# Kernel tuning notes

Hardware: AMD Instinct MI355X
Metric: run time of the kernel (lower is better)

The kernel has to match this reference:

```python
import jax, jax.numpy as jnp
import numpy as np

N_HEAD, CTX, N_EMBD, HEAD_SIZE = 16, 2048, 1024, 64
D_MODEL = N_HEAD * HEAD_SIZE  # 1024


def setup_inputs() -> dict:
    key = jax.random.key(0)
    ks = jax.random.split(key, 8)
    s_in = 1.0 / np.sqrt(N_EMBD)
    s_d = 1.0 / np.sqrt(D_MODEL)
    s_ff = 1.0 / np.sqrt(4 * D_MODEL)
    return {
        "x": jax.random.normal(ks[0], (4, CTX, N_EMBD), dtype=jnp.float32),
        # per-head q/k/v projections stacked over heads: [H, n_embd, head_size]
        "Wq": jax.random.normal(ks[1], (N_HEAD, N_EMBD, HEAD_SIZE), dtype=jnp.float32) * s_in,
        "Wk": jax.random.normal(ks[2], (N_HEAD, N_EMBD, HEAD_SIZE), dtype=jnp.float32) * s_in,
        "Wv": jax.random.normal(ks[3], (N_HEAD, N_EMBD, HEAD_SIZE), dtype=jnp.float32) * s_in,
        # FFN: Linear(d, 4d) -> Linear(4d, d) -> ReLU (dropout = identity in eval)
        "W1": jax.random.normal(ks[4], (D_MODEL, 4 * D_MODEL), dtype=jnp.float32) * s_d,
        "b1": jnp.zeros((4 * D_MODEL,), dtype=jnp.float32),
        "W2": jax.random.normal(ks[5], (4 * D_MODEL, D_MODEL), dtype=jnp.float32) * s_ff,
        "b2": jnp.zeros((D_MODEL,), dtype=jnp.float32),
    }


def reference(x, Wq, Wk, Wv, W1, b1, W2, b2):
    B, T, C = x.shape
    scale = 1.0 / np.sqrt(HEAD_SIZE)
    # project: [B,T,C] x [H,C,D] -> [B,H,T,D]
    q = jnp.einsum('btc,hcd->bhtd', x, Wq)
    k = jnp.einsum('btc,hcd->bhtd', x, Wk)
    v = jnp.einsum('btc,hcd->bhtd', x, Wv)
    # causal attention scores [B,H,T,T]
    wei = jnp.einsum('bhtd,bhsd->bhts', q, k) * scale
    causal = jnp.tril(jnp.ones((T, T), dtype=bool))
    wei = jnp.where(causal, wei, -jnp.inf)
    wei = jax.nn.softmax(wei, axis=-1)
    out = jnp.einsum('bhts,bhsd->bhtd', wei, v)
    # concat heads -> [B,T,H*D]
    out = out.transpose(0, 2, 1, 3).reshape(B, T, D_MODEL)
    # FFN: note original applies ReLU AFTER the second linear
    h = out @ W1 + b1
    h = h @ W2 + b2
    return jax.nn.relu(h)
```

## Files before the change

kernel.cpp:

```cpp
#include <hip/hip_runtime.h>
#include <hip/hip_bf16.h>

typedef unsigned short u16;
typedef unsigned int u32;
typedef short bf16x8 __attribute__((ext_vector_type(8)));
typedef float floatx4 __attribute__((ext_vector_type(4)));

#define CTX 2048
#define HEADSZ 64
#define NHEAD 16
#define DMODEL 1024
#define DFF 4096
#define MROWS 8192
#define C_SCALE 0.18033688011112042f

__device__ __forceinline__ u16 f2b(float f) {
  union { float f; u32 i; } x; x.f = f;
  u32 i = x.i;
  return (u16)((i + 0x7fffu + ((i >> 16) & 1u)) >> 16);
}
__device__ __forceinline__ u32 pack2(float a, float b) {
  return (u32)f2b(a) | ((u32)f2b(b) << 16);
}
__device__ __forceinline__ u32 cvtpk(float a, float b) {
  u32 r;
  asm("v_cvt_pk_bf16_f32 %0, %1, %2" : "=v"(r) : "v"(a), "v"(b));
  return r;
}
__device__ __forceinline__ float ex2(float x) {
#if __has_builtin(__builtin_amdgcn_exp2f)
  return __builtin_amdgcn_exp2f(x);
#else
  float r;
  asm("v_exp_f32 %0, %1" : "=v"(r) : "v"(x));
  return r;
#endif
}

__device__ __forceinline__ void gl2lds16(const u16* g, u16* l) {
  __builtin_amdgcn_global_load_lds(
      (const __attribute__((address_space(1))) void*)g,
      (__attribute__((address_space(3))) void*)l, 16, 0, 0);
}

__global__ __launch_bounds__(256) void cvt2(const float* __restrict__ x,
                                            u16* __restrict__ xb,
                                            const float* __restrict__ w1,
                                            u16* __restrict__ w1b) {
  int i = (blockIdx.x * 256 + threadIdx.x) * 4;
  if (i < MROWS * 1024) {
    float4 v = *(const float4*)(x + i);
    *(uint2*)(xb + i) = make_uint2(pack2(v.x, v.y), pack2(v.z, v.w));
  } else {
    int j = i - MROWS * 1024;
    float4 v = *(const float4*)(w1 + j);
    *(uint2*)(w1b + j) = make_uint2(pack2(v.x, v.y), pack2(v.z, v.w));
  }
}

__global__ void transpose_f32_bf16(const float* __restrict__ in, u16* __restrict__ out,
                                   int R, int C, long ibs, long obs) {
  __shared__ u16 tile[32][33];
  const float* ip = in + (size_t)blockIdx.z * ibs;
  u16* op = out + (size_t)blockIdx.z * obs;
  int c0 = blockIdx.x * 32, r0 = blockIdx.y * 32;
  int tx = threadIdx.x, ty = threadIdx.y;
#pragma unroll
  for (int i = 0; i < 32; i += 8)
    tile[ty + i][tx] = f2b(ip[(size_t)(r0 + ty + i) * C + (c0 + tx)]);
  __syncthreads();
#pragma unroll
  for (int i = 0; i < 32; i += 8)
    op[(size_t)(c0 + ty + i) * R + (r0 + tx)] = tile[tx][ty + i];
}

__global__ void transpose_qkv(const float* __restrict__ Wq, const float* __restrict__ Wk,
                              const float* __restrict__ Wv, u16* __restrict__ out) {
  __shared__ u16 tile[32][33];
  int z = blockIdx.z;
  int sec = z >> 4, hh = z & 15;
  const float* ip = (sec == 0 ? Wq : sec == 1 ? Wk : Wv) + (size_t)hh * 65536;
  u16* op = out + (size_t)(sec * 16 + hh) * 65536;
  int c0 = blockIdx.x * 32, r0 = blockIdx.y * 32;
  int tx = threadIdx.x, ty = threadIdx.y;
#pragma unroll
  for (int i = 0; i < 32; i += 8)
    tile[ty + i][tx] = f2b(ip[(size_t)(r0 + ty + i) * 64 + (c0 + tx)]);
  __syncthreads();
#pragma unroll
  for (int i = 0; i < 32; i += 8)
    op[(size_t)(c0 + ty + i) * 1024 + (r0 + tx)] = tile[tx][ty + i];
}

__global__ __launch_bounds__(256) void reduce_wf(const float* __restrict__ p,
                                                 u16* __restrict__ wft) {
  int i = (blockIdx.x * 256 + threadIdx.x) * 4;
  float4 s = *(const float4*)(p + i);
#pragma unroll
  for (int sp = 1; sp < 8; sp++) {
    float4 v = *(const float4*)(p + ((size_t)sp << 20) + i);
    s.x += v.x; s.y += v.y; s.z += v.z; s.w += v.w;
  }
  *(uint2*)(wft + i) = make_uint2(pack2(s.x, s.y), pack2(s.z, s.w));
}

__global__ __launch_bounds__(256) void bf_acc(const float* __restrict__ b1,
                                              const float* __restrict__ W2,
                                              float* __restrict__ bf) {
  int n = blockIdx.x * 256 + threadIdx.x;
  int f0 = blockIdx.y * 128;
  float s = 0.f;
  for (int f = 0; f < 128; f++) s += b1[f0 + f] * W2[(size_t)(f0 + f) * 1024 + n];
  atomicAdd(&bf[n], s);
}

template <int MODE>
__global__ __launch_bounds__(512, 4) void gemm128(
    const u16* __restrict__ A, const u16* __restrict__ Bt,
    const float* __restrict__ bias,
    void* __restrict__ o0v, void* __restrict__ o1v, void* __restrict__ o2v,
    int N, int Klen, int Kstride) {
  __shared__ __align__(16) u16 SH[32768];
  const int tid = threadIdx.x;
  const int quad = (tid >> 4) & 3, l15 = tid & 15;
  const int wave = tid >> 6;
  const int wr = wave >> 2, wc = wave & 3;

  const int id = blockIdx.x;
  int blockM, blockN, koff;
  if (MODE == 3) {
    blockM = (id & 7) << 7;
    blockN = ((id >> 3) & 3) << 8;
    koff = (id >> 5) << 9;
  } else {
    blockM = (((id & 7) << 3) | ((id >> 3) & 7)) << 7;
    blockN = (id >> 6) << 8;
    koff = 0;
  }

  const int crow = tid >> 2;
  const int cslot = (tid & 3) ^ (crow & 3);
  const u16* ap  = A + (size_t)(blockM + crow) * Kstride + koff + cslot * 8;
  const u16* bp0 = Bt + (size_t)(blockN + crow) * Kstride + koff + cslot * 8;
  const u16* bp1 = bp0 + (size_t)128 * Kstride;

  floatx4 acc[4][4];
#pragma unroll
  for (int i = 0; i < 4; i++)
#pragma unroll
    for (int j = 0; j < 4; j++) acc[i][j] = (floatx4){0.f, 0.f, 0.f, 0.f};

  const int nk = Klen >> 5;

  gl2lds16(ap, SH + tid * 8);
  gl2lds16(bp0, SH + 8192 + tid * 8);
  gl2lds16(bp1, SH + 8192 + 4096 + tid * 8);
  ap += 32; bp0 += 32; bp1 += 32;

  const int aoff = (wr * 64 + l15) * 64 + ((quad ^ (l15 & 3)) << 4);
  const int boff = (wc * 64 + l15) * 64 + ((quad ^ (l15 & 3)) << 4);

#pragma unroll 1
  for (int t = 0; t < nk; t++) {
    const int cur = t & 1, nxt = cur ^ 1;
    if (t + 1 < nk) {
      u16* An = SH + nxt * 4096;
      u16* Bn = SH + 8192 + nxt * 8192;
      gl2lds16(ap, An + tid * 8);
      gl2lds16(bp0, Bn + tid * 8);
      gl2lds16(bp1, Bn + 4096 + tid * 8);
      ap += 32; bp0 += 32; bp1 += 32;
      asm volatile("s_waitcnt vmcnt(3)" ::: "memory");
    } else {
      asm volatile("s_waitcnt vmcnt(0)" ::: "memory");
    }
    __builtin_amdgcn_s_barrier();
    const char* ab = (const char*)(SH + cur * 4096);
    const char* bb = (const char*)(SH + 8192 + cur * 8192);
    bf16x8 ar[4], br[4];
#pragma unroll
    for (int mf = 0; mf < 4; mf++)
      ar[mf] = *(const bf16x8*)(ab + mf * 1024 + aoff);
#pragma unroll
    for (int nf = 0; nf < 4; nf++)
      br[nf] = *(const bf16x8*)(bb + nf * 1024 + boff);
    asm volatile("s_waitcnt lgkmcnt(0)" ::: "memory");
    __builtin_amdgcn_s_setprio(1);
#pragma unroll
    for (int mf = 0; mf < 4; mf++)
#pragma unroll
      for (int nf = 0; nf < 4; nf++)
        acc[mf][nf] = __builtin_amdgcn_mfma_f32_16x16x32_bf16(ar[mf], br[nf], acc[mf][nf], 0, 0, 0);
    __builtin_amdgcn_s_setprio(0);
    __builtin_amdgcn_s_barrier();
  }

  const int m0 = blockM + wr * 64 + quad * 4;
  const int n0 = blockN + wc * 64 + l15;
  if (MODE == 0) {
    u16* o0 = (u16*)o0v; u16* o1 = (u16*)o1v; u16* o2 = (u16*)o2v;
    const int lane = tid & 63;
    const int n0w = blockN + wc * 64;
    const int sec = n0w >> 10, hh = (n0w >> 6) & 15;
    const int m0w = blockM + wr * 64;
    const int b = m0w >> 11, t0 = m0w & 2047;
    const int lr = lane >> 3, lc = lane & 7;
    u16* buf = SH + wave * 4096;
    if (sec < 2) {
      u16* dst = (sec == 0) ? o0 : o1;
      const float scl = (sec == 0) ? C_SCALE : 1.0f;
#pragma unroll
      for (int nf = 0; nf < 4; nf++)
#pragma unroll
        for (int mf = 0; mf < 4; mf++)
#pragma unroll
          for (int r = 0; r < 4; r++) {
            int row = mf * 16 + quad * 4 + r;
            int col2 = (nf * 16 + l15) ^ ((row & 7) << 3);
            buf[row * 64 + col2] = f2b(acc[mf][nf][r] * scl);
          }
      u16* base = dst + ((size_t)((b * 16 + hh) * 2048 + t0)) * 64 + lc * 8;
#pragma unroll
      for (int i = 0; i < 8; i++) {
        int row = i * 8 + lr;
        uint4 v = *(const uint4*)(buf + row * 64 + ((lc ^ lr) << 3));
        *(uint4*)(base + (size_t)row * 64) = v;
      }
    } else {
      u16* dstv = o2 + ((size_t)((b * 16 + hh) * 64)) * CTX + t0;
#pragma unroll
      for (int nf = 0; nf < 4; nf++)
#pragma unroll
        for (int mf = 0; mf < 4; mf++) {
          int dr = nf * 16 + l15;
          int tc = (mf * 16 + quad * 4) ^ ((dr & 7) << 3);
          *(uint2*)&buf[dr * 64 + tc] = make_uint2(
              pack2(acc[mf][nf][0], acc[mf][nf][1]),
              pack2(acc[mf][nf][2], acc[mf][nf][3]));
        }
#pragma unroll
      for (int i = 0; i < 8; i++) {
        int dr = i * 8 + lr;
        uint4 v = *(const uint4*)&buf[dr * 64 + ((lc * 8) ^ ((dr & 7) << 3))];
        *(uint4*)(dstv + (size_t)dr * CTX + lc * 8) = v;
      }
    }
  } else if (MODE == 2) {
    float* o0 = (float*)o0v;
    const float* bias2 = (const float*)o1v;
#pragma unroll
    for (int nf = 0; nf < 4; nf++) {
      int n = n0 + nf * 16;
      float bv = bias[n] + bias2[n];
#pragma unroll
      for (int mf = 0; mf < 4; mf++)
#pragma unroll
        for (int r = 0; r < 4; r++) {
          int m = m0 + mf * 16 + r;
          float v = acc[mf][nf][r] + bv;
          o0[(size_t)m * N + n] = v > 0.f ? v : 0.f;
        }
    }
  } else {
    float* o0 = (float*)o0v + ((size_t)(id >> 5) << 20);
#pragma unroll
    for (int nf = 0; nf < 4; nf++) {
      int n = n0 + nf * 16;
#pragma unroll
      for (int mf = 0; mf < 4; mf++)
#pragma unroll
        for (int r = 0; r < 4; r++) {
          int m = m0 + mf * 16 + r;
          o0[(size_t)m * N + n] = acc[mf][nf][r];
        }
    }
  }
}

__global__ __launch_bounds__(256) void attn_mfma(
    const u16* __restrict__ Q, const u16* __restrict__ K,
    const u16* __restrict__ Vt, u16* __restrict__ out) {
  __shared__ __align__(16) u16 Kbuf[2][4096];
  __shared__ __align__(16) u16 Vbuf[2][4096];
  __shared__ __align__(16) u16 Plds[4][32][72];
  const int tid = threadIdx.x;
  const int wave = tid >> 6, lane = tid & 63;
  const int quad = lane >> 4, l15 = lane & 15;
  const int sx = l15 & 7;
  const int bh = blockIdx.x;
  const int j = 15 - blockIdx.y;
  const size_t qkb = (size_t)bh * CTX * 64;
  const size_t vb = (size_t)bh * 64 * CTX;

  const int ch0 = wave * 64 + lane;
  const int ch1 = 256 + ch0;
  const int r0 = ch0 >> 3, s0 = (ch0 & 7) ^ (r0 & 7);
  const int r1 = ch1 >> 3, s1 = (ch1 & 7) ^ (r1 & 7);
  const u16* kg0 = K + qkb + r0 * 64 + s0 * 8;
  const u16* kg1 = K + qkb + r1 * 64 + s1 * 8;
  const u16* vg0 = Vt + vb + (size_t)r0 * CTX + s0 * 8;
  const u16* vg1 = Vt + vb + (size_t)r1 * CTX + s1 * 8;

  const int qbase = j * 128 + wave * 32;
  const int NST = 2 * j + 2;
  const int nstw = 2 * j + (wave >> 1) + 1;

  bf16x8 qf[2][2];
#pragma unroll
  for (int mt = 0; mt < 2; mt++)
#pragma unroll
    for (int kc = 0; kc < 2; kc++)
      qf[mt][kc] = *(const bf16x8*)(Q + qkb + (size_t)(qbase + mt * 16 + l15) * 64 + kc * 32 + quad * 8);

  bf16x8 ones;
#pragma unroll
  for (int i = 0; i < 8; i++) ones[i] = (short)0x3F80;

  floatx4 o[2][4];
#pragma unroll
  for (int mt = 0; mt < 2; mt++)
#pragma unroll
    for (int dt = 0; dt < 4; dt++) o[mt][dt] = (floatx4){0.f, 0.f, 0.f, 0.f};
  floatx4 lacc[2];
  lacc[0] = (floatx4){0.f, 0.f, 0.f, 0.f};
  lacc[1] = (floatx4){0.f, 0.f, 0.f, 0.f};

  gl2lds16(kg0, &Kbuf[0][wave * 512]);
  gl2lds16(kg1, &Kbuf[0][2048 + wave * 512]);
  gl2lds16(vg0, &Vbuf[0][wave * 512]);
  gl2lds16(vg1, &Vbuf[0][2048 + wave * 512]);

#pragma unroll 1
  for (int st = 0; st < NST; st++) {
    __syncthreads();
    if (st + 1 < NST) {
      const int sb = (st + 1) * 64;
      const int b = (st + 1) & 1;
      gl2lds16(kg0 + sb * 64, &Kbuf[b][wave * 512]);
      gl2lds16(kg1 + sb * 64, &Kbuf[b][2048 + wave * 512]);
      gl2lds16(vg0 + sb, &Vbuf[b][wave * 512]);
      gl2lds16(vg1 + sb, &Vbuf[b][2048 + wave * 512]);
    }
    if (st >= nstw) continue;
    const int sbase = st * 64;
    const u16* kb = Kbuf[st & 1];
    const u16* vv = Vbuf[st & 1];

    floatx4 stf[2][4];
    __builtin_amdgcn_s_setprio(1);
#pragma unroll
    for (int sc = 0; sc < 4; sc++) {
      const bf16x8* kr = (const bf16x8*)(kb + (sc * 16 + l15) * 64);
      bf16x8 k0 = kr[quad ^ sx];
      bf16x8 k1 = kr[(4 + quad) ^ sx];
#pragma unroll
      for (int mt = 0; mt < 2; mt++) {
        floatx4 z = (floatx4){0.f, 0.f, 0.f, 0.f};
        z = __builtin_amdgcn_mfma_f32_16x16x32_bf16(k0, qf[mt][0], z, 0, 0, 0);
        stf[mt][sc] = __builtin_amdgcn_mfma_f32_16x16x32_bf16(k1, qf[mt][1], z, 0, 0, 0);
      }
    }
    __builtin_amdgcn_s_setprio(0);
    if (st == nstw - 1) {
#pragma unroll
      for (int mt = 0; mt < 2; mt++) {
        int qq = qbase + mt * 16 + l15;
#pragma unroll
        for (int sc = 0; sc < 4; sc++)
#pragma unroll
          for (int r = 0; r < 4; r++) {
            int s = sbase + sc * 16 + quad * 4 + r;
            if (s > qq) stf[mt][sc][r] = -1e30f;
          }
      }
    }
#pragma unroll
    for (int mt = 0; mt < 2; mt++) {
#pragma unroll
      for (int sc = 0; sc < 4; sc++) {
        floatx4 s4 = stf[mt][sc];
        float p0 = ex2(s4[0]);
        float p1 = ex2(s4[1]);
        float p2 = ex2(s4[2]);
        float p3 = ex2(s4[3]);
        *(uint2*)&Plds[wave][mt * 16 + l15][sc * 16 + quad * 4] =
            make_uint2(cvtpk(p0, p1), cvtpk(p2, p3));
      }
    }
    asm volatile("s_waitcnt lgkmcnt(0)" ::: "memory");
    __builtin_amdgcn_s_setprio(1);
#pragma unroll
    for (int sc2 = 0; sc2 < 2; sc2++) {
      bf16x8 pf[2];
#pragma unroll
      for (int mt = 0; mt < 2; mt++)
        pf[mt] = *(const bf16x8*)&Plds[wave][mt * 16 + l15][sc2 * 32 + quad * 8];
#pragma unroll
      for (int mt = 0; mt < 2; mt++)
        lacc[mt] = __builtin_amdgcn_mfma_f32_16x16x32_bf16(ones, pf[mt], lacc[mt], 0, 0, 0);
#pragma unroll
      for (int dt = 0; dt < 4; dt++) {
        const bf16x8* vr = (const bf16x8*)(vv + (dt * 16 + l15) * 64);
        bf16x8 vf = vr[(sc2 * 4 + quad) ^ sx];
#pragma unroll
        for (int mt = 0; mt < 2; mt++)
          o[mt][dt] = __builtin_amdgcn_mfma_f32_16x16x32_bf16(vf, pf[mt], o[mt][dt], 0, 0, 0);
      }
    }
    __builtin_amdgcn_s_setprio(0);
  }

#pragma unroll
  for (int mt = 0; mt < 2; mt++) {
    float inv = 1.0f / lacc[mt][0];
    int row = (bh >> 4) * CTX + qbase + mt * 16 + l15;
    u16* orow = out + (size_t)row * DMODEL + (bh & 15) * 64;
#pragma unroll
    for (int dt = 0; dt < 4; dt++) {
      floatx4 v = o[mt][dt];
      *(u32*)(orow + dt * 16 + quad * 4) = cvtpk(v[0] * inv, v[1] * inv);
      *(u32*)(orow + dt * 16 + quad * 4 + 2) = cvtpk(v[2] * inv, v[3] * inv);
    }
  }
}

extern "C" void kernel_launch(void* const* d_in, const int* in_sizes, int n_in,
                              void* d_out, int out_size, void* d_ws, size_t ws_size,
                              hipStream_t stream) {
  const float* x  = (const float*)d_in[0];
  const float* Wq = (const float*)d_in[1];
  const float* Wk = (const float*)d_in[2];
  const float* Wv = (const float*)d_in[3];
  const float* W1 = (const float*)d_in[4];
  const float* b1 = (const float*)d_in[5];
  const float* W2 = (const float*)d_in[6];
  const float* b2 = (const float*)d_in[7];
  float* out = (float*)d_out;

  u16* ws    = (u16*)d_ws;
  u16* W2t   = ws;
  u16* W1b   = W2t + (size_t)1024 * 4096;
  u16* Wft   = W1b + (size_t)1024 * 4096;
  float* bfv = (float*)(Wft + (size_t)1024 * 1024);
  u16* xb    = Wft + (size_t)1024 * 1024 + 4096;
  u16* Wqkvt = xb + (size_t)MROWS * 1024;
  u16* q     = Wqkvt + (size_t)3072 * 1024;
  u16* k     = q + (size_t)MROWS * 1024;
  u16* vt    = k + (size_t)MROWS * 1024;
  u16* att   = xb;
  float* partials = (float*)q;

  cvt2<<<(MROWS * 1024 + 1024 * 4096) / 1024, 256, 0, stream>>>(x, xb, W1, W1b);

  dim3 tb(32, 8);
  transpose_qkv<<<dim3(2, 32, 48), tb, 0, stream>>>(Wq, Wk, Wv, Wqkvt);
  transpose_f32_bf16<<<dim3(32, 128, 1), tb, 0, stream>>>(W2, W2t, 4096, 1024, 0, 0);

  gemm128<3><<<256, 512, 0, stream>>>(W2t, W1b, nullptr, partials, nullptr, nullptr,
                                      1024, 512, 4096);
  reduce_wf<<<1024, 256, 0, stream>>>(partials, Wft);
  hipMemsetAsync(bfv, 0, 1024 * sizeof(float), stream);
  bf_acc<<<dim3(4, 32), 256, 0, stream>>>(b1, W2, bfv);

  gemm128<0><<<768, 512, 0, stream>>>(xb, Wqkvt, nullptr, q, k, vt, 3072, 1024, 1024);
  attn_mfma<<<dim3(64, 16), 256, 0, stream>>>(q, k, vt, att);
  gemm128<2><<<256, 512, 0, stream>>>(att, Wft, bfv, out, (void*)b2, nullptr,
                                      1024, 1024, 1024);
}
```

Baseline: 306.4 us.

## Merge prep kernels and co-schedule weight-fold GEMM with QKV projection

Folds the conversions, transposes and bias-fold into a single prep launch. The W2·W1 weight-fold GEMM now runs as extra blocks of the QKV projection launch, using split-K of 4 with K=1024 instead of 8 with K=512, and its partial reduction runs as an extra row of blocks in the attention launch. This removes many small launches and serial dependencies, and the partials get their own workspace instead of aliasing q. The bias-fold becomes a single serial 4096-long loop per thread in only 4 blocks, which may become a straggler in the prep kernel.

```diff
diff --git a/kernel.cpp b/kernel.cpp
--- a/kernel.cpp
+++ b/kernel.cpp
@@ -43,75 +43,58 @@
       (__attribute__((address_space(3))) void*)l, 16, 0, 0);
 }
 
-__global__ __launch_bounds__(256) void cvt2(const float* __restrict__ x,
-                                            u16* __restrict__ xb,
-                                            const float* __restrict__ w1,
-                                            u16* __restrict__ w1b) {
-  int i = (blockIdx.x * 256 + threadIdx.x) * 4;
-  if (i < MROWS * 1024) {
+__global__ __launch_bounds__(256) void prep(
+    const float* __restrict__ x, u16* __restrict__ xb,
+    const float* __restrict__ W1, u16* __restrict__ w1b,
+    const float* __restrict__ Wq, const float* __restrict__ Wk,
+    const float* __restrict__ Wv, u16* __restrict__ wqkvt,
+    const float* __restrict__ W2, u16* __restrict__ w2t,
+    const float* __restrict__ b1, const float* __restrict__ b2,
+    float* __restrict__ bfv) {
+  __shared__ u16 tile[32][33];
+  const int b = blockIdx.x;
+  const int tid = threadIdx.x;
+  if (b < 8192) {
+    int i = b * 1024 + tid * 4;
     float4 v = *(const float4*)(x + i);
     *(uint2*)(xb + i) = make_uint2(pack2(v.x, v.y), pack2(v.z, v.w));
+  } else if (b < 12288) {
+    int j = (b - 8192) * 1024 + tid * 4;
+    float4 v = *(const float4*)(W1 + j);
+    *(uint2*)(w1b + j) = make_uint2(pack2(v.x, v.y), pack2(v.z, v.w));
+  } else if (b < 15360) {
+    int bb = b - 12288;
+    int bx = bb & 1, by = (bb >> 1) & 31, z = bb >> 6;
+    int sec = z >> 4, hh = z & 15;
+    const float* ip = (sec == 0 ? Wq : sec == 1 ? Wk : Wv) + (size_t)hh * 65536;
+    u16* op = wqkvt + (size_t)(sec * 16 + hh) * 65536;
+    int c0 = bx * 32, r0 = by * 32;
+    int tx = tid & 31, ty = tid >> 5;
+#pragma unroll
+    for (int i = 0; i < 32; i += 8)
+      tile[ty + i][tx] = f2b(ip[(size_t)(r0 + ty + i) * 64 + (c0 + tx)]);
+    __syncthreads();
+#pragma unroll
+    for (int i = 0; i < 32; i += 8)
+      op[(size_t)(c0 + ty + i) * 1024 + (r0 + tx)] = tile[tx][ty + i];
+  } else if (b < 19456) {
+    int bb = b - 15360;
+    int bx = bb & 31, by = bb >> 5;
+    int c0 = bx * 32, r0 = by * 32;
+    int tx = tid & 31, ty = tid >> 5;
+#pragma unroll
+    for (int i = 0; i < 32; i += 8)
+      tile[ty + i][tx] = f2b(W2[(size_t)(r0 + ty + i) * 1024 + (c0 + tx)]);
+    __syncthreads();
+#pragma unroll
+    for (int i = 0; i < 32; i += 8)
+      w2t[(size_t)(c0 + ty + i) * 4096 + (r0 + tx)] = tile[tx][ty + i];
   } else {
-    int j = i - MROWS * 1024;
-    float4 v = *(const float4*)(w1 + j);
-    *(uint2*)(w1b + j) = make_uint2(pack2(v.x, v.y), pack2(v.z, v.w));
-  }
-}
-
-__global__ void transpose_f32_bf16(const float* __restrict__ in, u16* __restrict__ out,
-                                   int R, int C, long ibs, long obs) {
-  __shared__ u16 tile[32][33];
-  const float* ip = in + (size_t)blockIdx.z * ibs;
-  u16* op = out + (size_t)blockIdx.z * obs;
-  int c0 = blockIdx.x * 32, r0 = blockIdx.y * 32;
-  int tx = threadIdx.x, ty = threadIdx.y;
-#pragma unroll
-  for (int i = 0; i < 32; i += 8)
-    tile[ty + i][tx] = f2b(ip[(size_t)(r0 + ty + i) * C + (c0 + tx)]);
-  __syncthreads();
-#pragma unroll
-  for (int i = 0; i < 32; i += 8)
-    op[(size_t)(c0 + ty + i) * R + (r0 + tx)] = tile[tx][ty + i];
-}
-
-__global__ void transpose_qkv(const float* __restrict__ Wq, const float* __restrict__ Wk,
-                              const float* __restrict__ Wv, u16* __restrict__ out) {
-  __shared__ u16 tile[32][33];
-  int z = blockIdx.z;
-  int sec = z >> 4, hh = z & 15;
-  const float* ip = (sec == 0 ? Wq : sec == 1 ? Wk : Wv) + (size_t)hh * 65536;
-  u16* op = out + (size_t)(sec * 16 + hh) * 65536;
-  int c0 = blockIdx.x * 32, r0 = blockIdx.y * 32;
-  int tx = threadIdx.x, ty = threadIdx.y;
-#pragma unroll
-  for (int i = 0; i < 32; i += 8)
-    tile[ty + i][tx] = f2b(ip[(size_t)(r0 + ty + i) * 64 + (c0 + tx)]);
-  __syncthreads();
-#pragma unroll
-  for (int i = 0; i < 32; i += 8)
-    op[(size_t)(c0 + ty + i) * 1024 + (r0 + tx)] = tile[tx][ty + i];
-}
-
-__global__ __launch_bounds__(256) void reduce_wf(const float* __restrict__ p,
-                                                 u16* __restrict__ wft) {
-  int i = (blockIdx.x * 256 + threadIdx.x) * 4;
-  float4 s = *(const float4*)(p + i);
-#pragma unroll
-  for (int sp = 1; sp < 8; sp++) {
-    float4 v = *(const float4*)(p + ((size_t)sp << 20) + i);
-    s.x += v.x; s.y += v.y; s.z += v.z; s.w += v.w;
-  }
-  *(uint2*)(wft + i) = make_uint2(pack2(s.x, s.y), pack2(s.z, s.w));
-}
-
-__global__ __launch_bounds__(256) void bf_acc(const float* __restrict__ b1,
-                                              const float* __restrict__ W2,
-                                              float* __restrict__ bf) {
-  int n = blockIdx.x * 256 + threadIdx.x;
-  int f0 = blockIdx.y * 128;
-  float s = 0.f;
-  for (int f = 0; f < 128; f++) s += b1[f0 + f] * W2[(size_t)(f0 + f) * 1024 + n];
-  atomicAdd(&bf[n], s);
+    int n = (b - 19456) * 256 + tid;
+    float s = b2[n];
+    for (int f = 0; f < 4096; f++) s += b1[f] * W2[(size_t)f * 1024 + n];
+    bfv[n] = s;
+  }
 }
 
 template <int MODE>
@@ -119,7 +102,9 @@
     const u16* __restrict__ A, const u16* __restrict__ Bt,
     const float* __restrict__ bias,
     void* __restrict__ o0v, void* __restrict__ o1v, void* __restrict__ o2v,
-    int N, int Klen, int Kstride) {
+    int N, int Klen, int Kstride,
+    const u16* __restrict__ A2, const u16* __restrict__ B2t,
+    void* __restrict__ o3v) {
   __shared__ __align__(16) u16 SH[32768];
   const int tid = threadIdx.x;
   const int quad = (tid >> 4) & 3, l15 = tid & 15;
@@ -127,22 +112,30 @@
   const int wr = wave >> 2, wc = wave & 3;
 
   const int id = blockIdx.x;
-  int blockM, blockN, koff;
-  if (MODE == 3) {
-    blockM = (id & 7) << 7;
-    blockN = ((id >> 3) & 3) << 8;
-    koff = (id >> 5) << 9;
+  const bool wf = (MODE == 0) && (id >= 768);
+  const int id2 = id - 768;
+  int blockM, blockN, koff, Kl, Ks;
+  const u16* Ap;
+  const u16* Btp;
+  if (wf) {
+    blockM = (id2 & 7) << 7;
+    blockN = ((id2 >> 3) & 3) << 8;
+    koff = (id2 >> 5) << 10;
+    Kl = 1024; Ks = 4096;
+    Ap = A2; Btp = B2t;
   } else {
     blockM = (((id & 7) << 3) | ((id >> 3) & 7)) << 7;
     blockN = (id >> 6) << 8;
     koff = 0;
+    Kl = Klen; Ks = Kstride;
+    Ap = A; Btp = Bt;
   }
 
   const int crow = tid >> 2;
   const int cslot = (tid & 3) ^ (crow & 3);
-  const u16* ap  = A + (size_t)(blockM + crow) * Kstride + koff + cslot * 8;
-  const u16* bp0 = Bt + (size_t)(blockN + crow) * Kstride + koff + cslot * 8;
-  const u16* bp1 = bp0 + (size_t)128 * Kstride;
+  const u16* ap  = Ap + (size_t)(blockM + crow) * Ks + koff + cslot * 8;
+  const u16* bp0 = Btp + (size_t)(blockN + crow) * Ks + koff + cslot * 8;
+  const u16* bp1 = bp0 + (size_t)128 * Ks;
 
   floatx4 acc[4][4];
 #pragma unroll
@@ -150,7 +143,7 @@
 #pragma unroll
     for (int j = 0; j < 4; j++) acc[i][j] = (floatx4){0.f, 0.f, 0.f, 0.f};
 
-  const int nk = Klen >> 5;
+  const int nk = Kl >> 5;
 
   gl2lds16(ap, SH + tid * 8);
   gl2lds16(bp0, SH + 8192 + tid * 8);
@@ -197,7 +190,7 @@
 
   const int m0 = blockM + wr * 64 + quad * 4;
   const int n0 = blockN + wc * 64 + l15;
-  if (MODE == 0) {
+  if (MODE == 0 && !wf) {
     u16* o0 = (u16*)o0v; u16* o1 = (u16*)o1v; u16* o2 = (u16*)o2v;
     const int lane = tid & 63;
     const int n0w = blockN + wc * 64;
@@ -245,13 +238,25 @@
         *(uint4*)(dstv + (size_t)dr * CTX + lc * 8) = v;
       }
     }
-  } else if (MODE == 2) {
-    float* o0 = (float*)o0v;
-    const float* bias2 = (const float*)o1v;
+  } else if (MODE == 0) {
+    float* o3 = (float*)o3v + ((size_t)(id2 >> 5) << 20);
 #pragma unroll
     for (int nf = 0; nf < 4; nf++) {
       int n = n0 + nf * 16;
-      float bv = bias[n] + bias2[n];
+#pragma unroll
+      for (int mf = 0; mf < 4; mf++)
+#pragma unroll
+        for (int r = 0; r < 4; r++) {
+          int m = m0 + mf * 16 + r;
+          o3[(size_t)m * 1024 + n] = acc[mf][nf][r];
+        }
+    }
+  } else {
+    float* o0 = (float*)o0v;
+#pragma unroll
+    for (int nf = 0; nf < 4; nf++) {
+      int n = n0 + nf * 16;
+      float bv = bias[n];
 #pragma unroll
       for (int mf = 0; mf < 4; mf++)
 #pragma unroll
@@ -261,29 +266,32 @@
           o0[(size_t)m * N + n] = v > 0.f ? v : 0.f;
         }
     }
-  } else {
-    float* o0 = (float*)o0v + ((size_t)(id >> 5) << 20);
-#pragma unroll
-    for (int nf = 0; nf < 4; nf++) {
-      int n = n0 + nf * 16;
-#pragma unroll
-      for (int mf = 0; mf < 4; mf++)
-#pragma unroll
-        for (int r = 0; r < 4; r++) {
-          int m = m0 + mf * 16 + r;
-          o0[(size_t)m * N + n] = acc[mf][nf][r];
-        }
-    }
   }
 }
 
 __global__ __launch_bounds__(256) void attn_mfma(
     const u16* __restrict__ Q, const u16* __restrict__ K,
-    const u16* __restrict__ Vt, u16* __restrict__ out) {
+    const u16* __restrict__ Vt, u16* __restrict__ out,
+    const float* __restrict__ partials, u16* __restrict__ wft) {
   __shared__ __align__(16) u16 Kbuf[2][4096];
   __shared__ __align__(16) u16 Vbuf[2][4096];
   __shared__ __align__(16) u16 Plds[4][32][72];
   const int tid = threadIdx.x;
+  if (blockIdx.y == 16) {
+    int off = blockIdx.x * 16384;
+#pragma unroll 1
+    for (int it = 0; it < 16; it++) {
+      int i = off + (it * 256 + tid) * 4;
+      float4 s = *(const float4*)(partials + i);
+#pragma unroll
+      for (int sp = 1; sp < 4; sp++) {
+        float4 v = *(const float4*)(partials + ((size_t)sp << 20) + i);
+        s.x += v.x; s.y += v.y; s.z += v.z; s.w += v.w;
+      }
+      *(uint2*)(wft + i) = make_uint2(pack2(s.x, s.y), pack2(s.z, s.w));
+    }
+    return;
+  }
   const int wave = tid >> 6, lane = tid & 63;
   const int quad = lane >> 4, l15 = lane & 15;
   const int sx = l15 & 7;
@@ -447,23 +455,14 @@
   u16* q     = Wqkvt + (size_t)3072 * 1024;
   u16* k     = q + (size_t)MROWS * 1024;
   u16* vt    = k + (size_t)MROWS * 1024;
+  float* partials = (float*)(vt + (size_t)MROWS * 1024);
   u16* att   = xb;
-  float* partials = (float*)q;
-
-  cvt2<<<(MROWS * 1024 + 1024 * 4096) / 1024, 256, 0, stream>>>(x, xb, W1, W1b);
-
-  dim3 tb(32, 8);
-  transpose_qkv<<<dim3(2, 32, 48), tb, 0, stream>>>(Wq, Wk, Wv, Wqkvt);
-  transpose_f32_bf16<<<dim3(32, 128, 1), tb, 0, stream>>>(W2, W2t, 4096, 1024, 0, 0);
-
-  gemm128<3><<<256, 512, 0, stream>>>(W2t, W1b, nullptr, partials, nullptr, nullptr,
-                                      1024, 512, 4096);
-  reduce_wf<<<1024, 256, 0, stream>>>(partials, Wft);
-  hipMemsetAsync(bfv, 0, 1024 * sizeof(float), stream);
-  bf_acc<<<dim3(4, 32), 256, 0, stream>>>(b1, W2, bfv);
-
-  gemm128<0><<<768, 512, 0, stream>>>(xb, Wqkvt, nullptr, q, k, vt, 3072, 1024, 1024);
-  attn_mfma<<<dim3(64, 16), 256, 0, stream>>>(q, k, vt, att);
-  gemm128<2><<<256, 512, 0, stream>>>(att, Wft, bfv, out, (void*)b2, nullptr,
-                                      1024, 1024, 1024);
-}
+
+  prep<<<19460, 256, 0, stream>>>(x, xb, W1, W1b, Wq, Wk, Wv, Wqkvt,
+                                  W2, W2t, b1, b2, bfv);
+  gemm128<0><<<896, 512, 0, stream>>>(xb, Wqkvt, nullptr, q, k, vt,
+                                      3072, 1024, 1024, W2t, W1b, partials);
+  attn_mfma<<<dim3(64, 17), 256, 0, stream>>>(q, k, vt, att, partials, Wft);
+  gemm128<2><<<256, 512, 0, stream>>>(att, Wft, bfv, out, nullptr, nullptr,
+                                      1024, 1024, 1024, nullptr, nullptr, nullptr);
+}
```

Result: slower. 403.3 us (+31.6%).
